# Kernel tuning notes

Measured on AMD Instinct MI355X. Metric: run time of the kernel, lower is better.

Reference implementation:

```python
import jax, jax.numpy as jnp
import numpy as np

T, B, I, H, A = 2048, 2, 40, 44, 262144  # seq_len, batch, input, hidden, max action len
E = 2 * H  # 88, branch embedding dim; E + I == 128 (Linear in_features)


def setup_inputs() -> dict:
    key = jax.random.key(0)
    ks = jax.random.split(key, 11)
    s = 1.0 / np.sqrt(H).astype(np.float32)
    u = lambda k, shape: jax.random.uniform(k, shape, jnp.float32, -s, s)
    sl = 1.0 / np.sqrt(E + I).astype(np.float32)
    return {
        "x": jax.random.normal(ks[0], (T, B, I), jnp.float32),
        "h0": jax.random.normal(ks[1], (1, B, H), jnp.float32),
        "c0": jax.random.normal(ks[2], (1, B, H), jnp.float32),
        "action": jax.random.normal(ks[3], (B, A, I), jnp.float32),
        "act_length": jax.random.randint(ks[4], (B,), 1, A + 1, jnp.int32),
        "W_ih": u(ks[5], (4 * H, I)),
        "W_hh": u(ks[6], (4 * H, H)),
        "b_ih": u(ks[7], (4 * H,)),
        "b_hh": u(ks[8], (4 * H,)),
        "W_v": jax.random.uniform(ks[9], (1, E + I), jnp.float32, -sl, sl),
        "b_v": jax.random.uniform(ks[10], (1,), jnp.float32, -sl, sl),
    }


def _lstm_final(x, h0, c0, W_ih, W_hh, b_ih, b_hh):
    # single-layer LSTM, returns final (h, c), each (B, H); torch gate order i,f,g,o
    def step(carry, xt):
        h, c = carry
        g = xt @ W_ih.T + b_ih + h @ W_hh.T + b_hh  # (B, 4H)
        i, f, gg, o = jnp.split(g, 4, axis=-1)
        c = jax.nn.sigmoid(f) * c + jax.nn.sigmoid(i) * jnp.tanh(gg)
        h = jax.nn.sigmoid(o) * jnp.tanh(c)
        return (h, c), None
    (h, c), _ = jax.lax.scan(step, (h0[0], c0[0]), x)
    return h, c


def reference(x, h0, c0, action, act_length, W_ih, W_hh, b_ih, b_hh, W_v, b_v):
    h, c = _lstm_final(x, h0, c0, W_ih, W_hh, b_ih, b_hh)
    emb = jnp.concatenate([h, c], axis=-1)  # (B, 88) == brench_embeding[0]
    w = W_v[0]
    w_e, w_a = w[:E], w[E:]  # split Linear(128->1) weight over [embed | act]
    # val[b, i] = emb[b].w_e + action[b, i].w_a + b_v  (fused ragged linear)
    vals = (emb @ w_e)[:, None] + jnp.einsum("bad,d->ba", action, w_a) + b_v[0]
    mask = jnp.arange(A)[None, :] < act_length[:, None]  # ragged lengths
    return jnp.where(mask, vals, 0.0)
```

## Files before the change

kernel.cpp:

```cpp
#include <hip/hip_runtime.h>

typedef float v2f __attribute__((ext_vector_type(2)));
typedef float v4f __attribute__((ext_vector_type(4)));

#define T_STEPS 2048
#define BATCH   2
#define IDIM    40
#define HDIM    44
#define GDIM    176
#define ADIM    262144
#define EDIM    88
#define NEG_L   (-1.4426950408889634f)
#define NEG_2L  (-2.8853900817779268f)

__global__ __launch_bounds__(192) void xproj_kernel(
    const float* __restrict__ x,
    const float* __restrict__ W_ih,
    const float* __restrict__ b_ih,
    const float* __restrict__ b_hh,
    float* __restrict__ xproj)
{
    const int tb = blockIdx.x;
    const int gi = threadIdx.x;
    __shared__ __align__(16) float xs[IDIM];
    if (threadIdx.x < IDIM) xs[threadIdx.x] = x[(size_t)tb * IDIM + threadIdx.x];
    __syncthreads();
    if (gi < GDIM) {
        const float* wr = W_ih + gi * IDIM;
        float a0 = 0.f, a1 = 0.f;
        #pragma unroll
        for (int i = 0; i < IDIM; i += 4) {
            float4 wv = *(const float4*)&wr[i];
            float4 xv = *(const float4*)&xs[i];
            a0 += wv.x * xv.x + wv.z * xv.z;
            a1 += wv.y * xv.y + wv.w * xv.w;
        }
        const float scale = (gi >= 2 * HDIM && gi < 3 * HDIM) ? NEG_2L : NEG_L;
        xproj[(size_t)tb * GDIM + gi] = scale * (a0 + a1 + b_ih[gi] + b_hh[gi]);
    }
}

__global__ __launch_bounds__(128)
__attribute__((amdgpu_waves_per_eu(1, 1)))
void lstm_kernel(
    const float* __restrict__ xproj,
    const float* __restrict__ h0,
    const float* __restrict__ c0,
    const float* __restrict__ W_hh,
    const float* __restrict__ W_v,
    const float* __restrict__ b_v,
    float* __restrict__ base_out)
{
    const int b    = blockIdx.x;
    const int tid  = threadIdx.x;
    const int wave = tid >> 6;
    const int lane = tid & 63;
    const int sub  = lane & 31;
    const int half = lane >> 5;
    const bool act = (sub < 22);
    const int subc = act ? sub : 21;
    const int unit = wave * 22 + subc;

    __shared__ __align__(16) float hsh[2][64];
    __shared__ float part[2];

    const int row0 = half ? (2 * HDIM + unit) : unit;
    const int row1 = row0 + HDIM;
    const float sc0 = half ? NEG_2L : NEG_L;
    const float sc1 = NEG_L;

    v2f w0[22], w1[22];
    {
        const float* r0p = W_hh + (size_t)row0 * HDIM;
        const float* r1p = W_hh + (size_t)row1 * HDIM;
        #pragma unroll
        for (int k = 0; k < 22; ++k) {
            w0[k] = ((const v2f*)r0p)[k] * sc0;
            w1[k] = ((const v2f*)r1p)[k] * sc1;
        }
    }

    float c = c0[b * HDIM + unit];
    if (tid < HDIM) hsh[0][tid] = h0[b * HDIM + tid];
    if (tid >= HDIM && tid < 64) hsh[0][tid] = 0.f;
    __syncthreads();

    v2f hp[22];
    #pragma unroll
    for (int k = 0; k < 11; ++k) {
        v4f t = ((const v4f*)hsh[0])[k];
        hp[2 * k]     = __builtin_shufflevector(t, t, 0, 1);
        hp[2 * k + 1] = __builtin_shufflevector(t, t, 2, 3);
    }

    const float* xp = xproj + (size_t)b * GDIM;
    #define LDX(d0, d1, s) { const float* _a = xp + (size_t)(s) * (BATCH * GDIM); \
        d0 = _a[row0]; d1 = _a[row1]; }
    float r0v, r1v, p0v, p1v;
    LDX(r0v, r1v, 0) LDX(p0v, p1v, 1)

    float hval = 0.f;

    #pragma unroll 1
    for (int step = 0; step < T_STEPS; ++step) {
        v2f a0 = {r0v, 0.f}, a1 = {r1v, 0.f};
        #pragma unroll
        for (int k = 0; k < 22; ++k) {
            a0 = __builtin_elementwise_fma(w0[k], hp[k], a0);
            a1 = __builtin_elementwise_fma(w1[k], hp[k], a1);
        }
        float y0 = a0.x + a0.y;
        float y1 = a1.x + a1.y;

        float v0 = __builtin_amdgcn_rcpf(1.0f + __builtin_amdgcn_exp2f(y0));
        float v1 = __builtin_amdgcn_rcpf(1.0f + __builtin_amdgcn_exp2f(y1));

        float o0 = __shfl_xor(v0, 32);
        float o1 = __shfl_xor(v1, 32);

        float s_i = half ? o0 : v0;
        float s_f = half ? o1 : v1;
        float w_g = half ? v0 : o0;
        float s_o = half ? v1 : o1;

        float t_g = __builtin_fmaf(2.0f, w_g, -1.0f);
        c = s_f * c + s_i * t_g;
        float w_c = __builtin_amdgcn_rcpf(1.0f + __builtin_amdgcn_exp2f(c * NEG_2L));
        hval = __builtin_fmaf(s_o + s_o, w_c, -s_o);

        const int wb = (step + 1) & 1;
        hsh[wb][unit] = hval;
        __syncthreads();

        #pragma unroll
        for (int k = 0; k < 11; ++k) {
            v4f t = ((const v4f*)hsh[wb])[k];
            hp[2 * k]     = __builtin_shufflevector(t, t, 0, 1);
            hp[2 * k + 1] = __builtin_shufflevector(t, t, 2, 3);
        }

        r0v = p0v; r1v = p1v;
        const int ns = (step + 2 < T_STEPS) ? step + 2 : (T_STEPS - 1);
        LDX(p0v, p1v, ns)
    }
    #undef LDX

    float p = 0.f;
    if (act && half == 0) p = hval * W_v[unit] + c * W_v[HDIM + unit];
    #pragma unroll
    for (int off = 32; off; off >>= 1) p += __shfl_down(p, off);
    if (lane == 0) part[wave] = p;
    __syncthreads();
    if (tid == 0) base_out[b] = part[0] + part[1] + b_v[0];
}

__global__ __launch_bounds__(256) void action_kernel(
    const float* __restrict__ action,
    const int*   __restrict__ act_length,
    const float* __restrict__ W_v,
    const float* __restrict__ base,
    float* __restrict__ out)
{
    const int idx = blockIdx.x * 256 + threadIdx.x;
    const int b = idx >> 18;
    const int a = idx & (ADIM - 1);
    if (a >= act_length[b]) { out[idx] = 0.f; return; }
    const float* row = action + (size_t)idx * IDIM;
    float a0 = 0.f, a1 = 0.f;
    #pragma unroll
    for (int i = 0; i < IDIM; i += 4) {
        float4 av = *(const float4*)&row[i];
        a0 += av.x * W_v[EDIM + i + 0] + av.z * W_v[EDIM + i + 2];
        a1 += av.y * W_v[EDIM + i + 1] + av.w * W_v[EDIM + i + 3];
    }
    out[idx] = base[b] + a0 + a1;
}

extern "C" void kernel_launch(void* const* d_in, const int* in_sizes, int n_in,
                              void* d_out, int out_size, void* d_ws, size_t ws_size,
                              hipStream_t stream) {
    const float* x        = (const float*)d_in[0];
    const float* h0       = (const float*)d_in[1];
    const float* c0       = (const float*)d_in[2];
    const float* action   = (const float*)d_in[3];
    const int*   act_len  = (const int*)  d_in[4];
    const float* W_ih     = (const float*)d_in[5];
    const float* W_hh     = (const float*)d_in[6];
    const float* b_ih     = (const float*)d_in[7];
    const float* b_hh     = (const float*)d_in[8];
    const float* W_v      = (const float*)d_in[9];
    const float* b_v      = (const float*)d_in[10];
    float* out = (float*)d_out;

    float* xproj = (float*)d_ws;
    float* base  = xproj + (size_t)T_STEPS * BATCH * GDIM;

    xproj_kernel<<<dim3(T_STEPS * BATCH), dim3(192), 0, stream>>>(
        x, W_ih, b_ih, b_hh, xproj);
    lstm_kernel<<<dim3(BATCH), dim3(128), 0, stream>>>(
        xproj, h0, c0, W_hh, W_v, b_v, base);
    action_kernel<<<dim3((BATCH * ADIM) / 256), dim3(256), 0, stream>>>(
        action, act_len, W_v, base, out);
}
```

Before: 637.6 us.

## Overlap action projection with serial LSTM recurrence in one launch

```diff
diff --git a/kernel.cpp b/kernel.cpp
--- a/kernel.cpp
+++ b/kernel.cpp
@@ -12,6 +12,7 @@
 #define EDIM    88
 #define NEG_L   (-1.4426950408889634f)
 #define NEG_2L  (-2.8853900817779268f)
+#define NACT_BLK 4096
 
 __global__ __launch_bounds__(192) void xproj_kernel(
     const float* __restrict__ x,
@@ -42,15 +43,31 @@
 
 __global__ __launch_bounds__(128)
 __attribute__((amdgpu_waves_per_eu(1, 1)))
-void lstm_kernel(
+void lstm_action_kernel(
     const float* __restrict__ xproj,
     const float* __restrict__ h0,
     const float* __restrict__ c0,
     const float* __restrict__ W_hh,
     const float* __restrict__ W_v,
     const float* __restrict__ b_v,
-    float* __restrict__ base_out)
+    float* __restrict__ base_out,
+    const float* __restrict__ action,
+    float* __restrict__ out)
 {
+    if (blockIdx.x >= BATCH) {
+        const int idx = (blockIdx.x - BATCH) * 128 + threadIdx.x;
+        const float* row = action + (size_t)idx * IDIM;
+        float a0 = 0.f, a1 = 0.f;
+        #pragma unroll
+        for (int i = 0; i < IDIM; i += 4) {
+            float4 av = *(const float4*)&row[i];
+            a0 += av.x * W_v[EDIM + i + 0] + av.z * W_v[EDIM + i + 2];
+            a1 += av.y * W_v[EDIM + i + 1] + av.w * W_v[EDIM + i + 3];
+        }
+        out[idx] = a0 + a1;
+        return;
+    }
+
     const int b    = blockIdx.x;
     const int tid  = threadIdx.x;
     const int wave = tid >> 6;
@@ -101,48 +118,50 @@
 
     float hval = 0.f;
 
+    #define STEP(WB, NS) { \
+        v2f a0 = {r0v, 0.f}, a1 = {r1v, 0.f}; \
+        _Pragma("unroll") \
+        for (int k = 0; k < 22; ++k) { \
+            a0 = __builtin_elementwise_fma(w0[k], hp[k], a0); \
+            a1 = __builtin_elementwise_fma(w1[k], hp[k], a1); \
+        } \
+        float y0 = a0.x + a0.y; \
+        float y1 = a1.x + a1.y; \
+        float v0 = __builtin_amdgcn_rcpf(1.0f + __builtin_amdgcn_exp2f(y0)); \
+        float v1 = __builtin_amdgcn_rcpf(1.0f + __builtin_amdgcn_exp2f(y1)); \
+         \
+         \
+        float sx1 = v0, sy1 = v1; \
+        asm("v_permlane32_swap_b32 %0, %1" : "+v"(sx1), "+v"(sy1)); \
+        float sx2 = v1, sy2 = v0; \
+        asm("v_permlane32_swap_b32 %0, %1" : "+v"(sx2), "+v"(sy2)); \
+        float s_i = half ? sx2 : v0; \
+        float s_f = half ? sx1 : v1; \
+        float w_g = half ? v0 : sy1; \
+        float s_o = half ? v1 : sy2; \
+        float t_g = __builtin_fmaf(2.0f, w_g, -1.0f); \
+        c = s_f * c + s_i * t_g; \
+        float w_c = __builtin_amdgcn_rcpf(1.0f + __builtin_amdgcn_exp2f(c * NEG_2L)); \
+        hval = __builtin_fmaf(s_o + s_o, w_c, -s_o); \
+        hsh[WB][unit] = hval; \
+        __syncthreads(); \
+        _Pragma("unroll") \
+        for (int k = 0; k < 11; ++k) { \
+            v4f t = ((const v4f*)hsh[WB])[k]; \
+            hp[2 * k]     = __builtin_shufflevector(t, t, 0, 1); \
+            hp[2 * k + 1] = __builtin_shufflevector(t, t, 2, 3); \
+        } \
+        r0v = p0v; r1v = p1v; \
+        const int _ns = ((NS) < T_STEPS) ? (NS) : (T_STEPS - 1); \
+        LDX(p0v, p1v, _ns) \
+    }
+
     #pragma unroll 1
-    for (int step = 0; step < T_STEPS; ++step) {
-        v2f a0 = {r0v, 0.f}, a1 = {r1v, 0.f};
-        #pragma unroll
-        for (int k = 0; k < 22; ++k) {
-            a0 = __builtin_elementwise_fma(w0[k], hp[k], a0);
-            a1 = __builtin_elementwise_fma(w1[k], hp[k], a1);
-        }
-        float y0 = a0.x + a0.y;
-        float y1 = a1.x + a1.y;
-
-        float v0 = __builtin_amdgcn_rcpf(1.0f + __builtin_amdgcn_exp2f(y0));
-        float v1 = __builtin_amdgcn_rcpf(1.0f + __builtin_amdgcn_exp2f(y1));
-
-        float o0 = __shfl_xor(v0, 32);
-        float o1 = __shfl_xor(v1, 32);
-
-        float s_i = half ? o0 : v0;
-        float s_f = half ? o1 : v1;
-        float w_g = half ? v0 : o0;
-        float s_o = half ? v1 : o1;
-
-        float t_g = __builtin_fmaf(2.0f, w_g, -1.0f);
-        c = s_f * c + s_i * t_g;
-        float w_c = __builtin_amdgcn_rcpf(1.0f + __builtin_amdgcn_exp2f(c * NEG_2L));
-        hval = __builtin_fmaf(s_o + s_o, w_c, -s_o);
-
-        const int wb = (step + 1) & 1;
-        hsh[wb][unit] = hval;
-        __syncthreads();
-
-        #pragma unroll
-        for (int k = 0; k < 11; ++k) {
-            v4f t = ((const v4f*)hsh[wb])[k];
-            hp[2 * k]     = __builtin_shufflevector(t, t, 0, 1);
-            hp[2 * k + 1] = __builtin_shufflevector(t, t, 2, 3);
-        }
-
-        r0v = p0v; r1v = p1v;
-        const int ns = (step + 2 < T_STEPS) ? step + 2 : (T_STEPS - 1);
-        LDX(p0v, p1v, ns)
-    }
+    for (int step = 0; step < T_STEPS; step += 2) {
+        STEP(1, step + 2)
+        STEP(0, step + 3)
+    }
+    #undef STEP
     #undef LDX
 
     float p = 0.f;
@@ -154,26 +173,16 @@
     if (tid == 0) base_out[b] = part[0] + part[1] + b_v[0];
 }
 
-__global__ __launch_bounds__(256) void action_kernel(
-    const float* __restrict__ action,
+__global__ __launch_bounds__(256) void finalize_kernel(
     const int*   __restrict__ act_length,
-    const float* __restrict__ W_v,
     const float* __restrict__ base,
     float* __restrict__ out)
 {
     const int idx = blockIdx.x * 256 + threadIdx.x;
     const int b = idx >> 18;
     const int a = idx & (ADIM - 1);
-    if (a >= act_length[b]) { out[idx] = 0.f; return; }
-    const float* row = action + (size_t)idx * IDIM;
-    float a0 = 0.f, a1 = 0.f;
-    #pragma unroll
-    for (int i = 0; i < IDIM; i += 4) {
-        float4 av = *(const float4*)&row[i];
-        a0 += av.x * W_v[EDIM + i + 0] + av.z * W_v[EDIM + i + 2];
-        a1 += av.y * W_v[EDIM + i + 1] + av.w * W_v[EDIM + i + 3];
-    }
-    out[idx] = base[b] + a0 + a1;
+    const float v = out[idx];
+    out[idx] = (a < act_length[b]) ? v + base[b] : 0.f;
 }
 
 extern "C" void kernel_launch(void* const* d_in, const int* in_sizes, int n_in,
@@ -197,8 +206,8 @@
 
     xproj_kernel<<<dim3(T_STEPS * BATCH), dim3(192), 0, stream>>>(
         x, W_ih, b_ih, b_hh, xproj);
-    lstm_kernel<<<dim3(BATCH), dim3(128), 0, stream>>>(
-        xproj, h0, c0, W_hh, W_v, b_v, base);
-    action_kernel<<<dim3((BATCH * ADIM) / 256), dim3(256), 0, stream>>>(
-        action, act_len, W_v, base, out);
-}
+    lstm_action_kernel<<<dim3(BATCH + NACT_BLK), dim3(128), 0, stream>>>(
+        xproj, h0, c0, W_hh, W_v, b_v, base, action, out);
+    finalize_kernel<<<dim3((BATCH * ADIM) / 256), dim3(256), 0, stream>>>(
+        act_len, base, out);
+}
```

Result: faster. 565.1 us (median of 2 runs) (-11.4%).
